# Optimization experiments

Measured on AMD Instinct MI355X. Metric: run time of the kernel, lower is better.

## Reference

```python
import jax, jax.numpy as jnp
import numpy as np

N = 65536          # rays per batch
NC = 64            # coarse samples (config.num_samples_coarse)
NF = 128           # fine samples (config.num_samples_fine)
NEAR, FAR = 0.1, 1000.0


def setup_inputs() -> dict:
    key = jax.random.key(0)
    k = jax.random.split(key, 7)
    ray_origins = jax.random.normal(k[0], (N, 3), jnp.float32)
    ray_directions = jax.random.normal(k[1], (N, 3), jnp.float32)
    # stratified coarse t_vals == sample_points_along_rays(stratified=True)
    t = NEAR + (FAR - NEAR) * jnp.linspace(0.0, 1.0, NC, dtype=jnp.float32)
    t = jnp.broadcast_to(t, (N, NC))
    mids = 0.5 * (t[:, 1:] + t[:, :-1])
    upper = jnp.concatenate([mids, t[:, -1:]], axis=-1)
    lower = jnp.concatenate([t[:, :1], mids], axis=-1)
    t_rand = jax.random.uniform(k[2], (N, NC), jnp.float32)
    coarse_t_vals = lower + (upper - lower) * t_rand
    coarse_weights = jax.random.uniform(k[3], (N, NC), jnp.float32)
    u = jax.random.uniform(k[4], (N, NF), jnp.float32)
    colors = jax.random.uniform(k[5], (N, NC + NF, 3), jnp.float32)
    densities = jax.random.uniform(k[6], (N, NC + NF, 1), jnp.float32)
    return {"ray_origins": ray_origins, "ray_directions": ray_directions,
            "coarse_weights": coarse_weights, "coarse_t_vals": coarse_t_vals,
            "u": u, "colors": colors, "densities": densities}


def _hierarchical_sampling(ray_origins, ray_directions, coarse_weights, coarse_t_vals, u):
    # inverse-CDF importance resampling (GridNeRFRenderer.hierarchical_sampling)
    w = coarse_weights + 1e-5
    pdf = w / jnp.sum(w, axis=-1, keepdims=True)                 # [N, NC]
    cdf = jnp.cumsum(pdf, axis=-1)
    cdf = jnp.concatenate([jnp.zeros_like(cdf[..., :1]), cdf], axis=-1)  # [N, NC+1]
    # per-ray searchsorted (right)
    indices = jax.vmap(lambda c, uu: jnp.searchsorted(c, uu, side="right"))(cdf, u)  # [N, NF]
    nc = coarse_t_vals.shape[-1]
    below = jnp.clip(indices - 1, 0, nc - 1)
    above = jnp.clip(indices, 0, nc - 1)
    cdf_b = jnp.take_along_axis(cdf, below, axis=1)
    cdf_a = jnp.take_along_axis(cdf, above, axis=1)
    t_b = jnp.take_along_axis(coarse_t_vals, below, axis=1)
    t_a = jnp.take_along_axis(coarse_t_vals, above, axis=1)
    denom = cdf_a - cdf_b
    denom = jnp.where(denom < 1e-5, jnp.ones_like(denom), denom)
    tt = (u - cdf_b) / denom
    fine_t_vals = t_b + tt * (t_a - t_b)
    combined_t_vals = jnp.sort(jnp.concatenate([coarse_t_vals, fine_t_vals], axis=-1), axis=-1)  # [N, NC+NF]
    fine_points = ray_origins[:, None, :] + ray_directions[:, None, :] * combined_t_vals[..., None]
    return fine_points, combined_t_vals


def _volume_rendering(colors, densities, t_vals, ray_directions):
    dists = t_vals[..., 1:] - t_vals[..., :-1]
    dists = jnp.concatenate([dists, jnp.full_like(dists[..., :1], 1e10)], axis=-1)
    dists = dists * jnp.linalg.norm(ray_directions, axis=-1, keepdims=True)   # [N, S]
    alpha = 1.0 - jnp.exp(-densities[..., 0] * dists)                         # [N, S]
    # exclusive cumprod transmittance (== cumprod + roll + T[...,0]=1)
    trans = jnp.cumprod(1.0 - alpha + 1e-10, axis=-1)
    trans = jnp.concatenate([jnp.ones_like(trans[..., :1]), trans[..., :-1]], axis=-1)
    weights = alpha * trans
    rgb = jnp.sum(weights[..., None] * colors, axis=-2)   # [N, 3]
    depth = jnp.sum(weights * t_vals, axis=-1)            # [N]
    opacity = jnp.sum(weights, axis=-1)                   # [N]
    return rgb, depth, opacity, weights


def reference(ray_origins, ray_directions, coarse_weights, coarse_t_vals, u, colors, densities):
    fine_points, combined_t_vals = _hierarchical_sampling(
        ray_origins, ray_directions, coarse_weights, coarse_t_vals, u)
    rgb, depth, opacity, weights = _volume_rendering(
        colors, densities, combined_t_vals, ray_directions)
    return (rgb, depth, opacity, fine_points)
```

## Files before the change

### kernel.cpp

```cpp
#include <hip/hip_runtime.h>
#include <math.h>


#define NRAYS 65536
#define NCC   64
#define NFF   128
#define SS    192

struct f3 { float x, y, z; };

__global__ __launch_bounds__(256)
void nerf_fused(const float* __restrict__ ro,  const float* __restrict__ rd,
                const float* __restrict__ cw,  const float* __restrict__ ct,
                const float* __restrict__ uu,  const float* __restrict__ col,
                const float* __restrict__ den, float* __restrict__ out)
{
    const int lane = threadIdx.x & 63;
    const int wv   = threadIdx.x >> 6;
    const int ray  = blockIdx.x * 4 + wv;

    __shared__ float s_cdf[4][65];
    __shared__ float s_ct [4][64];
    __shared__ float s_su [4][128];
    __shared__ float s_vals[4][192];

    float wt = cw[(size_t)ray * NCC + lane] + 1e-5f;
    float tc = ct[(size_t)ray * NCC + lane];
    float2 u2 = *(const float2*)(uu + (size_t)ray * NFF + 2 * lane);
    float dx = rd[(size_t)ray * 3 + 0], dy = rd[(size_t)ray * 3 + 1], dz = rd[(size_t)ray * 3 + 2];
    float ox = ro[(size_t)ray * 3 + 0], oy = ro[(size_t)ray * 3 + 1], oz = ro[(size_t)ray * 3 + 2];
    f3 dn = *(const f3*)(den + (size_t)ray * SS + 3 * lane);
    const float* cp = col + (size_t)ray * (SS * 3) + 9 * lane;
    f3 c0 = *(const f3*)(cp + 0);
    f3 c1 = *(const f3*)(cp + 3);
    f3 c2 = *(const f3*)(cp + 6);

    float x = wt;
    #pragma unroll
    for (int off = 1; off < 64; off <<= 1) {
        float y = __shfl_up(x, off);
        if (lane >= off) x += y;
    }
    float total = __shfl(x, 63);
    float cv = x / total;
    #pragma unroll
    for (int off = 1; off < 64; off <<= 1) {
        float y = __shfl_up(cv, off);
        if (lane >= off) cv = fmaxf(cv, y);
    }
    s_cdf[wv][lane + 1] = cv;
    if (lane == 0) s_cdf[wv][0] = 0.0f;
    s_ct[wv][lane] = tc;

    float v0 = u2.x, v1 = u2.y;
    #pragma unroll
    for (int k = 2; k <= 128; k <<= 1) {
        #pragma unroll
        for (int j = k >> 1; j >= 1; j >>= 1) {
            bool up = (((lane << 1) & k) == 0);
            if (j == 1) {
                float a = v0, b = v1;
                v0 = up ? fminf(a, b) : fmaxf(a, b);
                v1 = up ? fmaxf(a, b) : fminf(a, b);
            } else {
                int m = j >> 1;
                bool keepmin = (((lane & m) == 0) == up);
                float p0 = __shfl_xor(v0, m);
                float p1 = __shfl_xor(v1, m);
                v0 = keepmin ? fminf(v0, p0) : fmaxf(v0, p0);
                v1 = keepmin ? fminf(v1, p1) : fmaxf(v1, p1);
            }
        }
    }
    *(float2*)&s_su[wv][2 * lane] = make_float2(v0, v1);

    const float* cdfp = s_cdf[wv];
    const float* ctp  = s_ct[wv];
    float us[2] = {v0, v1};
    #pragma unroll
    for (int q = 0; q < 2; ++q) {
        float u = us[q];
        int pos = 0;
        #pragma unroll
        for (int st = 32; st >= 1; st >>= 1) {
            int np = pos + st;
            pos = (cdfp[np] <= u) ? np : pos;
        }
        int above = (pos + 1 < 63) ? (pos + 1) : 63;
        float cb = cdfp[pos], ca = cdfp[above];
        float tb = ctp[pos],  ta = ctp[above];
        float dnm = ca - cb;
        dnm = (dnm < 1e-5f) ? 1.0f : dnm;
        float tt = (u - cb) / dnm;
        float fval = tb + tt * (ta - tb);
        int rank = 2 * lane + q + pos + 1;
        s_vals[wv][rank] = fval;
    }

    const float* sup = s_su[wv];
    float key = cdfp[lane];
    int cnt = 0;
    #pragma unroll
    for (int st = 128; st >= 1; st >>= 1) {
        int np = cnt + st;
        bool ok = (np <= 128) && (sup[np - 1] < key);
        cnt = ok ? np : cnt;
    }
    s_vals[wv][lane + cnt] = tc;

    float v0s = s_vals[wv][3 * lane + 0];
    float v1s = s_vals[wv][3 * lane + 1];
    float v2s = s_vals[wv][3 * lane + 2];

    float nrm = sqrtf(dx * dx + dy * dy + dz * dz);

    float tnext = __shfl_down(v0s, 1);
    float d0 = v1s - v0s;
    float d1 = v2s - v1s;
    float d2 = (lane == 63) ? 1e10f : (tnext - v2s);

    float e0 = __expf(-dn.x * (d0 * nrm));
    float e1 = __expf(-dn.y * (d1 * nrm));
    float e2 = __expf(-dn.z * (d2 * nrm));
    float a0 = 1.0f - e0, a1 = 1.0f - e1, a2 = 1.0f - e2;
    float f0 = e0 + 1e-10f, f1 = e1 + 1e-10f, f2 = e2 + 1e-10f;

    {
        float* fp = out + (size_t)5 * NRAYS + (size_t)ray * (SS * 3) + 9 * lane;
        f3 p0 = {ox + dx * v0s, oy + dy * v0s, oz + dz * v0s};
        f3 p1 = {ox + dx * v1s, oy + dy * v1s, oz + dz * v1s};
        f3 p2 = {ox + dx * v2s, oy + dy * v2s, oz + dz * v2s};
        ((f3*)fp)[0] = p0;
        ((f3*)fp)[1] = p1;
        ((f3*)fp)[2] = p2;
    }

    float pr1 = f0, pr2 = f0 * f1;
    float sx = pr2 * f2;
    #pragma unroll
    for (int off = 1; off < 64; off <<= 1) {
        float y = __shfl_up(sx, off);
        if (lane >= off) sx *= y;
    }
    float excl = __shfl_up(sx, 1);
    if (lane == 0) excl = 1.0f;
    float w0 = a0 * excl;
    float w1 = a1 * (excl * pr1);
    float w2 = a2 * (excl * pr2);

    float rr  = w0 * c0.x + w1 * c1.x + w2 * c2.x;
    float gg  = w0 * c0.y + w1 * c1.y + w2 * c2.y;
    float bb  = w0 * c0.z + w1 * c1.z + w2 * c2.z;
    float dep = w0 * v0s + w1 * v1s + w2 * v2s;
    float opa = w0 + w1 + w2;

    #pragma unroll
    for (int off = 32; off >= 1; off >>= 1) {
        rr  += __shfl_xor(rr,  off);
        gg  += __shfl_xor(gg,  off);
        bb  += __shfl_xor(bb,  off);
        dep += __shfl_xor(dep, off);
        opa += __shfl_xor(opa, off);
    }
    if (lane == 0) {
        out[(size_t)ray * 3 + 0] = rr;
        out[(size_t)ray * 3 + 1] = gg;
        out[(size_t)ray * 3 + 2] = bb;
        out[(size_t)3 * NRAYS + ray] = dep;
        out[(size_t)4 * NRAYS + ray] = opa;
    }
}

extern "C" void kernel_launch(void* const* d_in, const int* in_sizes, int n_in,
                              void* d_out, int out_size, void* d_ws, size_t ws_size,
                              hipStream_t stream) {
    const float* ro  = (const float*)d_in[0];
    const float* rd  = (const float*)d_in[1];
    const float* cw  = (const float*)d_in[2];
    const float* ct  = (const float*)d_in[3];
    const float* uu  = (const float*)d_in[4];
    const float* col = (const float*)d_in[5];
    const float* den = (const float*)d_in[6];
    float* out = (float*)d_out;
    (void)in_sizes; (void)n_in; (void)out_size; (void)d_ws; (void)ws_size;
    nerf_fused<<<NRAYS / 4, 256, 0, stream>>>(ro, rd, cw, ct, uu, col, den, out);
}
```

Measured before the change: 345.1 us.

## Process two rays per wavefront with 32-lane halves and more elements per lane

Each wavefront now handles two rays, one per 32-lane half, so every lane owns twice as many samples: 2 coarse weights, 4 fine u values and 6 combined samples. The bitonic sort, prefix scans, transmittance product and reductions use width-32 shuffles with more in-register work, and loads are widened to float2/float4. The goal is fewer cross-lane shuffle stages per sample and more per-thread ILP, at the cost of higher register pressure. The color load also moves later, after the transmittance scan.

```diff
diff --git a/kernel.cpp b/kernel.cpp
--- a/kernel.cpp
+++ b/kernel.cpp
@@ -17,68 +17,85 @@
 {
     const int lane = threadIdx.x & 63;
     const int wv   = threadIdx.x >> 6;
-    const int ray  = blockIdx.x * 4 + wv;
-
-    __shared__ float s_cdf[4][65];
-    __shared__ float s_ct [4][64];
-    __shared__ float s_su [4][128];
-    __shared__ float s_vals[4][192];
-
-    float wt = cw[(size_t)ray * NCC + lane] + 1e-5f;
-    float tc = ct[(size_t)ray * NCC + lane];
-    float2 u2 = *(const float2*)(uu + (size_t)ray * NFF + 2 * lane);
+    const int half = lane >> 5;
+    const int hl   = lane & 31;
+    const int ridx = wv * 2 + half;
+    const int ray  = blockIdx.x * 8 + ridx;
+
+    __shared__ float s_cdf [8][65];
+    __shared__ float s_ct  [8][64];
+    __shared__ float s_su  [8][128];
+    __shared__ float s_vals[8][192];
+
+    float2 cw2 = *(const float2*)(cw + (size_t)ray * NCC + 2 * hl);
+    float2 ct2 = *(const float2*)(ct + (size_t)ray * NCC + 2 * hl);
+    float4 u4  = *(const float4*)(uu + (size_t)ray * NFF + 4 * hl);
     float dx = rd[(size_t)ray * 3 + 0], dy = rd[(size_t)ray * 3 + 1], dz = rd[(size_t)ray * 3 + 2];
     float ox = ro[(size_t)ray * 3 + 0], oy = ro[(size_t)ray * 3 + 1], oz = ro[(size_t)ray * 3 + 2];
-    f3 dn = *(const f3*)(den + (size_t)ray * SS + 3 * lane);
-    const float* cp = col + (size_t)ray * (SS * 3) + 9 * lane;
-    f3 c0 = *(const f3*)(cp + 0);
-    f3 c1 = *(const f3*)(cp + 3);
-    f3 c2 = *(const f3*)(cp + 6);
-
-    float x = wt;
-    #pragma unroll
-    for (int off = 1; off < 64; off <<= 1) {
-        float y = __shfl_up(x, off);
-        if (lane >= off) x += y;
-    }
-    float total = __shfl(x, 63);
-    float cv = x / total;
-    #pragma unroll
-    for (int off = 1; off < 64; off <<= 1) {
-        float y = __shfl_up(cv, off);
-        if (lane >= off) cv = fmaxf(cv, y);
-    }
-    s_cdf[wv][lane + 1] = cv;
-    if (lane == 0) s_cdf[wv][0] = 0.0f;
-    s_ct[wv][lane] = tc;
-
-    float v0 = u2.x, v1 = u2.y;
-    #pragma unroll
-    for (int k = 2; k <= 128; k <<= 1) {
-        #pragma unroll
-        for (int j = k >> 1; j >= 1; j >>= 1) {
-            bool up = (((lane << 1) & k) == 0);
-            if (j == 1) {
-                float a = v0, b = v1;
-                v0 = up ? fminf(a, b) : fmaxf(a, b);
-                v1 = up ? fmaxf(a, b) : fminf(a, b);
-            } else {
-                int m = j >> 1;
-                bool keepmin = (((lane & m) == 0) == up);
-                float p0 = __shfl_xor(v0, m);
-                float p1 = __shfl_xor(v1, m);
-                v0 = keepmin ? fminf(v0, p0) : fmaxf(v0, p0);
-                v1 = keepmin ? fminf(v1, p1) : fmaxf(v1, p1);
-            }
-        }
-    }
-    *(float2*)&s_su[wv][2 * lane] = make_float2(v0, v1);
-
-    const float* cdfp = s_cdf[wv];
-    const float* ctp  = s_ct[wv];
-    float us[2] = {v0, v1};
-    #pragma unroll
-    for (int q = 0; q < 2; ++q) {
+    const float* dnp = den + (size_t)ray * SS + 6 * hl;
+    float2 dnA = *(const float2*)(dnp + 0);
+    float2 dnB = *(const float2*)(dnp + 2);
+    float2 dnC = *(const float2*)(dnp + 4);
+
+    float wt0 = cw2.x + 1e-5f, wt1 = cw2.y + 1e-5f;
+    float x = wt0 + wt1;
+    #pragma unroll
+    for (int off = 1; off < 32; off <<= 1) {
+        float y = __shfl_up(x, off, 32);
+        x += (hl >= off) ? y : 0.0f;
+    }
+    float total = __shfl(x, 31, 32);
+    float inv = 1.0f / total;
+    float cdfv1 = x * inv;
+    float cdfv0 = (x - wt1) * inv;
+    float pm = cdfv1;
+    #pragma unroll
+    for (int off = 1; off < 32; off <<= 1) {
+        float y = __shfl_up(pm, off, 32);
+        pm = fmaxf(pm, (hl >= off) ? y : 0.0f);
+    }
+    float mex = __shfl_up(pm, 1, 32);
+    mex = (hl == 0) ? 0.0f : mex;
+    float c0m = fmaxf(cdfv0, mex);
+    float c1m = fmaxf(cdfv1, c0m);
+    s_cdf[ridx][2 * hl + 1] = c0m;
+    s_cdf[ridx][2 * hl + 2] = c1m;
+    if (hl == 0) s_cdf[ridx][0] = 0.0f;
+    *(float2*)&s_ct[ridx][2 * hl] = ct2;
+
+    float v0 = u4.x, v1 = u4.y, v2 = u4.z, v3 = u4.w;
+
+#define LSTAGE(m, up) { \
+    bool km = ((hl & (m)) == 0) == (up); float p; \
+    p = __shfl_xor(v0, (m), 32); v0 = km ? fminf(v0, p) : fmaxf(v0, p); \
+    p = __shfl_xor(v1, (m), 32); v1 = km ? fminf(v1, p) : fmaxf(v1, p); \
+    p = __shfl_xor(v2, (m), 32); v2 = km ? fminf(v2, p) : fmaxf(v2, p); \
+    p = __shfl_xor(v3, (m), 32); v3 = km ? fminf(v3, p) : fmaxf(v3, p); }
+#define ISTAGE2(up) { float mn, mx; \
+    mn = fminf(v0, v2); mx = fmaxf(v0, v2); v0 = (up) ? mn : mx; v2 = (up) ? mx : mn; \
+    mn = fminf(v1, v3); mx = fmaxf(v1, v3); v1 = (up) ? mn : mx; v3 = (up) ? mx : mn; }
+#define ISTAGE1(up) { float mn, mx; \
+    mn = fminf(v0, v1); mx = fmaxf(v0, v1); v0 = (up) ? mn : mx; v1 = (up) ? mx : mn; \
+    mn = fminf(v2, v3); mx = fmaxf(v2, v3); v2 = (up) ? mn : mx; v3 = (up) ? mx : mn; }
+
+    {
+        float mn = fminf(v0, v1), mx = fmaxf(v0, v1); v0 = mn; v1 = mx;
+        mn = fminf(v2, v3); mx = fmaxf(v2, v3); v2 = mx; v3 = mn;
+    }
+    { bool up = ((hl & 1)  == 0); ISTAGE2(up); ISTAGE1(up); }
+    { bool up = ((hl & 2)  == 0); LSTAGE(1, up); ISTAGE2(up); ISTAGE1(up); }
+    { bool up = ((hl & 4)  == 0); LSTAGE(2, up); LSTAGE(1, up); ISTAGE2(up); ISTAGE1(up); }
+    { bool up = ((hl & 8)  == 0); LSTAGE(4, up); LSTAGE(2, up); LSTAGE(1, up); ISTAGE2(up); ISTAGE1(up); }
+    { bool up = ((hl & 16) == 0); LSTAGE(8, up); LSTAGE(4, up); LSTAGE(2, up); LSTAGE(1, up); ISTAGE2(up); ISTAGE1(up); }
+    { const bool up = true;       LSTAGE(16, up); LSTAGE(8, up); LSTAGE(4, up); LSTAGE(2, up); LSTAGE(1, up); ISTAGE2(up); ISTAGE1(up); }
+
+    *(float4*)&s_su[ridx][4 * hl] = make_float4(v0, v1, v2, v3);
+
+    const float* cdfp = s_cdf[ridx];
+    const float* ctp  = s_ct[ridx];
+    float us[4] = {v0, v1, v2, v3};
+    #pragma unroll
+    for (int q = 0; q < 4; ++q) {
         float u = us[q];
         int pos = 0;
         #pragma unroll
@@ -93,82 +110,103 @@
         dnm = (dnm < 1e-5f) ? 1.0f : dnm;
         float tt = (u - cb) / dnm;
         float fval = tb + tt * (ta - tb);
-        int rank = 2 * lane + q + pos + 1;
-        s_vals[wv][rank] = fval;
-    }
-
-    const float* sup = s_su[wv];
-    float key = cdfp[lane];
-    int cnt = 0;
+        int rank = 4 * hl + q + pos + 1;
+        s_vals[ridx][rank] = fval;
+    }
+
+    const float* sup = s_su[ridx];
+    float keyhi = c0m;
+    float keylo = __shfl_up(c1m, 1, 32);
+    keylo = (hl == 0) ? 0.0f : keylo;
+    int cnt0 = 0, cnt1 = 0;
     #pragma unroll
     for (int st = 128; st >= 1; st >>= 1) {
-        int np = cnt + st;
-        bool ok = (np <= 128) && (sup[np - 1] < key);
-        cnt = ok ? np : cnt;
-    }
-    s_vals[wv][lane + cnt] = tc;
-
-    float v0s = s_vals[wv][3 * lane + 0];
-    float v1s = s_vals[wv][3 * lane + 1];
-    float v2s = s_vals[wv][3 * lane + 2];
+        int np0 = cnt0 + st; bool ok0 = (np0 <= 128) && (sup[np0 - 1] < keylo); cnt0 = ok0 ? np0 : cnt0;
+        int np1 = cnt1 + st; bool ok1 = (np1 <= 128) && (sup[np1 - 1] < keyhi); cnt1 = ok1 ? np1 : cnt1;
+    }
+    s_vals[ridx][2 * hl     + cnt0] = ct2.x;
+    s_vals[ridx][2 * hl + 1 + cnt1] = ct2.y;
+
+    float2 a01 = *(const float2*)&s_vals[ridx][6 * hl + 0];
+    float2 a23 = *(const float2*)&s_vals[ridx][6 * hl + 2];
+    float2 a45 = *(const float2*)&s_vals[ridx][6 * hl + 4];
+    float sv[6] = {a01.x, a01.y, a23.x, a23.y, a45.x, a45.y};
 
     float nrm = sqrtf(dx * dx + dy * dy + dz * dz);
-
-    float tnext = __shfl_down(v0s, 1);
-    float d0 = v1s - v0s;
-    float d1 = v2s - v1s;
-    float d2 = (lane == 63) ? 1e10f : (tnext - v2s);
-
-    float e0 = __expf(-dn.x * (d0 * nrm));
-    float e1 = __expf(-dn.y * (d1 * nrm));
-    float e2 = __expf(-dn.z * (d2 * nrm));
-    float a0 = 1.0f - e0, a1 = 1.0f - e1, a2 = 1.0f - e2;
-    float f0 = e0 + 1e-10f, f1 = e1 + 1e-10f, f2 = e2 + 1e-10f;
+    float tnext = __shfl_down(sv[0], 1, 32);
+    float dd[6];
+    dd[0] = sv[1] - sv[0];
+    dd[1] = sv[2] - sv[1];
+    dd[2] = sv[3] - sv[2];
+    dd[3] = sv[4] - sv[3];
+    dd[4] = sv[5] - sv[4];
+    dd[5] = (hl == 31) ? 1e10f : (tnext - sv[5]);
+
+    float dnv[6] = {dnA.x, dnA.y, dnB.x, dnB.y, dnC.x, dnC.y};
+    float aa[6], ffv[6];
+    #pragma unroll
+    for (int r = 0; r < 6; ++r) {
+        float e = __expf(-dnv[r] * (dd[r] * nrm));
+        aa[r]  = 1.0f - e;
+        ffv[r] = e + 1e-10f;
+    }
 
     {
-        float* fp = out + (size_t)5 * NRAYS + (size_t)ray * (SS * 3) + 9 * lane;
-        f3 p0 = {ox + dx * v0s, oy + dy * v0s, oz + dz * v0s};
-        f3 p1 = {ox + dx * v1s, oy + dy * v1s, oz + dz * v1s};
-        f3 p2 = {ox + dx * v2s, oy + dy * v2s, oz + dz * v2s};
-        ((f3*)fp)[0] = p0;
-        ((f3*)fp)[1] = p1;
-        ((f3*)fp)[2] = p2;
-    }
-
-    float pr1 = f0, pr2 = f0 * f1;
-    float sx = pr2 * f2;
-    #pragma unroll
-    for (int off = 1; off < 64; off <<= 1) {
-        float y = __shfl_up(sx, off);
-        if (lane >= off) sx *= y;
-    }
-    float excl = __shfl_up(sx, 1);
-    if (lane == 0) excl = 1.0f;
-    float w0 = a0 * excl;
-    float w1 = a1 * (excl * pr1);
-    float w2 = a2 * (excl * pr2);
-
-    float rr  = w0 * c0.x + w1 * c1.x + w2 * c2.x;
-    float gg  = w0 * c0.y + w1 * c1.y + w2 * c2.y;
-    float bb  = w0 * c0.z + w1 * c1.z + w2 * c2.z;
-    float dep = w0 * v0s + w1 * v1s + w2 * v2s;
-    float opa = w0 + w1 + w2;
-
-    #pragma unroll
-    for (int off = 32; off >= 1; off >>= 1) {
-        rr  += __shfl_xor(rr,  off);
-        gg  += __shfl_xor(gg,  off);
-        bb  += __shfl_xor(bb,  off);
-        dep += __shfl_xor(dep, off);
-        opa += __shfl_xor(opa, off);
-    }
-    if (lane == 0) {
+        float* fp = out + (size_t)5 * NRAYS + (size_t)ray * (SS * 3) + 18 * hl;
+        #pragma unroll
+        for (int r = 0; r < 6; ++r) {
+            f3 p = {ox + dx * sv[r], oy + dy * sv[r], oz + dz * sv[r]};
+            ((f3*)fp)[r] = p;
+        }
+    }
+
+    float pr1 = ffv[0];
+    float pr2 = pr1 * ffv[1];
+    float pr3 = pr2 * ffv[2];
+    float pr4 = pr3 * ffv[3];
+    float pr5 = pr4 * ffv[4];
+    float sx  = pr5 * ffv[5];
+    #pragma unroll
+    for (int off = 1; off < 32; off <<= 1) {
+        float y = __shfl_up(sx, off, 32);
+        sx *= (hl >= off) ? y : 1.0f;
+    }
+    float excl = __shfl_up(sx, 1, 32);
+    excl = (hl == 0) ? 1.0f : excl;
+    float w0 = aa[0] * excl;
+    float w1 = aa[1] * (excl * pr1);
+    float w2 = aa[2] * (excl * pr2);
+    float w3 = aa[3] * (excl * pr3);
+    float w4 = aa[4] * (excl * pr4);
+    float w5 = aa[5] * (excl * pr5);
+
+    const f3* cp = (const f3*)(col + (size_t)ray * (SS * 3) + 18 * hl);
+    f3 c0 = cp[0], c1 = cp[1], c2 = cp[2], c3 = cp[3], c4 = cp[4], c5 = cp[5];
+
+    float rr  = w0*c0.x + w1*c1.x + w2*c2.x + w3*c3.x + w4*c4.x + w5*c5.x;
+    float gg  = w0*c0.y + w1*c1.y + w2*c2.y + w3*c3.y + w4*c4.y + w5*c5.y;
+    float bb  = w0*c0.z + w1*c1.z + w2*c2.z + w3*c3.z + w4*c4.z + w5*c5.z;
+    float dep = w0*sv[0] + w1*sv[1] + w2*sv[2] + w3*sv[3] + w4*sv[4] + w5*sv[5];
+    float opa = w0 + w1 + w2 + w3 + w4 + w5;
+
+    #pragma unroll
+    for (int off = 16; off >= 1; off >>= 1) {
+        rr  += __shfl_xor(rr,  off, 32);
+        gg  += __shfl_xor(gg,  off, 32);
+        bb  += __shfl_xor(bb,  off, 32);
+        dep += __shfl_xor(dep, off, 32);
+        opa += __shfl_xor(opa, off, 32);
+    }
+    if (hl == 0) {
         out[(size_t)ray * 3 + 0] = rr;
         out[(size_t)ray * 3 + 1] = gg;
         out[(size_t)ray * 3 + 2] = bb;
         out[(size_t)3 * NRAYS + ray] = dep;
         out[(size_t)4 * NRAYS + ray] = opa;
     }
+#undef LSTAGE
+#undef ISTAGE2
+#undef ISTAGE1
 }
 
 extern "C" void kernel_launch(void* const* d_in, const int* in_sizes, int n_in,
@@ -183,5 +221,5 @@
     const float* den = (const float*)d_in[6];
     float* out = (float*)d_out;
     (void)in_sizes; (void)n_in; (void)out_size; (void)d_ws; (void)ws_size;
-    nerf_fused<<<NRAYS / 4, 256, 0, stream>>>(ro, rd, cw, ct, uu, col, den, out);
+    nerf_fused<<<NRAYS / 8, 256, 0, stream>>>(ro, rd, cw, ct, uu, col, den, out);
 }
```

After: 373.1 us. 1.08x slower.
